# Kernel tuning notes

Hardware: AMD Instinct MI355X
Metric: run time of the kernel (lower is better)

## Reference

```python
import jax, jax.numpy as jnp
import numpy as np

B, S, IN, D, H, FF, L = 16, 1000, 32, 512, 8, 2048, 6
DK = D // H
EPS = 1e-5


def setup_inputs() -> dict:
    key = jax.random.key(0)
    ks = iter(jax.random.split(key, 64))
    def w(shape, s=0.02):
        return jax.random.normal(next(ks), shape, dtype=jnp.float32) * s
    inp = {
        'x': jax.random.normal(next(ks), (B, S, IN), dtype=jnp.float32),
        # input projection
        'Win': w((IN, D)), 'b_in': jnp.zeros((D,), jnp.float32),
        # per-layer attention weights (stacked over L layers)
        'Wq': w((L, D, D)), 'bq': jnp.zeros((L, D), jnp.float32),
        'Wk': w((L, D, D)), 'bk': jnp.zeros((L, D), jnp.float32),
        'Wv': w((L, D, D)), 'bv': jnp.zeros((L, D), jnp.float32),
        'Wo': w((L, D, D)), 'bo': jnp.zeros((L, D), jnp.float32),
        # per-layer feed-forward
        'W1': w((L, D, FF)), 'b1': jnp.zeros((L, FF), jnp.float32),
        'W2': w((L, FF, D)), 'b2': jnp.zeros((L, D), jnp.float32),
        # per-layer layernorms
        'ln1_g': jnp.ones((L, D), jnp.float32), 'ln1_b': jnp.zeros((L, D), jnp.float32),
        'ln2_g': jnp.ones((L, D), jnp.float32), 'ln2_b': jnp.zeros((L, D), jnp.float32),
        # final encoder norm
        'lnf_g': jnp.ones((D,), jnp.float32), 'lnf_b': jnp.zeros((D,), jnp.float32),
        # feature extraction head: D -> D/2 -> D/4
        'Wf1': w((D, D // 2)), 'bf1': jnp.zeros((D // 2,), jnp.float32),
        'Wf2': w((D // 2, D // 4)), 'bf2': jnp.zeros((D // 4,), jnp.float32),
        # reconstruction head: D/4 -> D/2 -> D -> IN
        'Wr1': w((D // 4, D // 2)), 'br1': jnp.zeros((D // 2,), jnp.float32),
        'Wr2': w((D // 2, D)), 'br2': jnp.zeros((D,), jnp.float32),
        'Wr3': w((D, IN)), 'br3': jnp.zeros((IN,), jnp.float32),
        # anomaly head: D/4 -> D/8 -> 1
        'Wa1': w((D // 4, D // 8)), 'ba1': jnp.zeros((D // 8,), jnp.float32),
        'Wa2': w((D // 8, 1)), 'ba2': jnp.zeros((1,), jnp.float32),
    }
    return inp


def _layernorm(x, g, b):
    m = jnp.mean(x, axis=-1, keepdims=True)
    v = jnp.var(x, axis=-1, keepdims=True)
    return (x - m) * jax.lax.rsqrt(v + EPS) * g + b


def _pos_encoding(seq_len, d_model):
    pos = jnp.arange(seq_len, dtype=jnp.float32)[:, None]
    div = jnp.exp(jnp.arange(0, d_model, 2, dtype=jnp.float32) * (-np.log(10000.0) / d_model))
    pe = jnp.zeros((seq_len, d_model), jnp.float32)
    pe = pe.at[:, 0::2].set(jnp.sin(pos * div))
    pe = pe.at[:, 1::2].set(jnp.cos(pos * div))
    return pe


def _encoder(h, Wq, bq, Wk, bk, Wv, bv, Wo, bo, W1, b1, W2, b2,
             ln1_g, ln1_b, ln2_g, ln2_b, lnf_g, lnf_b):
    h = h + _pos_encoding(h.shape[1], D)[None]
    scale = 1.0 / np.sqrt(DK)
    for i in range(L):
        # multi-head self-attention
        q = (h @ Wq[i] + bq[i]).reshape(B, S, H, DK).transpose(0, 2, 1, 3)
        k = (h @ Wk[i] + bk[i]).reshape(B, S, H, DK).transpose(0, 2, 1, 3)
        v = (h @ Wv[i] + bv[i]).reshape(B, S, H, DK).transpose(0, 2, 1, 3)
        scores = jnp.einsum('bhsd,bhtd->bhst', q, k) * scale  # [B,H,S,S]
        attn = jax.nn.softmax(scores, axis=-1)
        ctx = jnp.einsum('bhst,bhtd->bhsd', attn, v)
        ctx = ctx.transpose(0, 2, 1, 3).reshape(B, S, D)
        attn_out = ctx @ Wo[i] + bo[i]
        h = _layernorm(h + attn_out, ln1_g[i], ln1_b[i])
        # feed-forward
        ff = jax.nn.relu(h @ W1[i] + b1[i]) @ W2[i] + b2[i]
        h = _layernorm(h + ff, ln2_g[i], ln2_b[i])
    return _layernorm(h, lnf_g, lnf_b)


def reference(x, Win, b_in, Wq, bq, Wk, bk, Wv, bv, Wo, bo, W1, b1, W2, b2,
              ln1_g, ln1_b, ln2_g, ln2_b, lnf_g, lnf_b,
              Wf1, bf1, Wf2, bf2, Wr1, br1, Wr2, br2, Wr3, br3,
              Wa1, ba1, Wa2, ba2):
    h = x @ Win + b_in  # [B,S,D]
    h = _encoder(h, Wq, bq, Wk, bk, Wv, bv, Wo, bo, W1, b1, W2, b2,
                 ln1_g, ln1_b, ln2_g, ln2_b, lnf_g, lnf_b)
    feat = jax.nn.relu(h @ Wf1 + bf1) @ Wf2 + bf2  # [B,S,D/4]
    recon = jax.nn.relu(jax.nn.relu(feat @ Wr1 + br1) @ Wr2 + br2) @ Wr3 + br3  # [B,S,IN]
    anomaly = jax.nn.sigmoid(jax.nn.relu(feat @ Wa1 + ba1) @ Wa2 + ba2)  # [B,S,1]
    return recon, anomaly
```

## Files before the change

kernel.cpp:

```cpp
#include <hip/hip_runtime.h>
#include <hip/hip_bf16.h>
#include <math.h>

#define B_  16
#define S_  1000
#define IN_ 32
#define D_  512
#define H_  8
#define FF_ 2048
#define L_  6
#define DK_ 64
#define M_  (B_ * S_)
#define SP_ 1024

typedef __bf16 bf16x8 __attribute__((ext_vector_type(8)));
typedef float  floatx4 __attribute__((ext_vector_type(4)));

#define FLAG_RELU 1
#define FLAG_BF16 2
#define FLAG_QKV  4

#define QSCALE 0.18033688011112042f

__device__ __forceinline__ void gll16(const __bf16* g, __bf16* l) {
    __builtin_amdgcn_global_load_lds(
        (const __attribute__((address_space(1))) unsigned int*)g,
        (__attribute__((address_space(3))) unsigned int*)l, 16, 0, 0);
}

__global__ __launch_bounds__(256) void gemm_mfma(
    const __bf16* __restrict__ A, const __bf16* __restrict__ BT,
    const float* __restrict__ bias, void* __restrict__ C,
    int M, int N, int K, int flags)
{
    __shared__ __bf16 Asm[128 * 32];
    __shared__ __bf16 Bsm[128 * 32];

    int tid  = threadIdx.x;
    int wave = tid >> 6;
    int lane = tid & 63;
    int bm = blockIdx.y * 128;
    int bn = blockIdx.x * 128;
    int wm = (wave & 1) * 64;
    int wn = (wave >> 1) * 64;
    int lm = lane & 15;
    int lq = lane >> 4;

    floatx4 acc[4][4] = {};

    int crow  = tid >> 2;
    int cpart = (tid & 3) * 8;
    const __bf16* ag0 = A + (size_t)(bm + crow) * K + cpart;
    const __bf16* ag1 = A + (size_t)(bm + 64 + crow) * K + cpart;
    __bf16* al0 = Asm + tid * 8;
    __bf16* al1 = Asm + 2048 + tid * 8;
    int nr0 = bn + crow, nr1 = bn + 64 + crow;
    const __bf16* bg0 = BT + (size_t)nr0 * K + cpart;
    const __bf16* bg1 = BT + (size_t)nr1 * K + cpart;
    __bf16* bl0 = Bsm + tid * 8;
    __bf16* bl1 = Bsm + 2048 + tid * 8;
    bool bv0 = nr0 < N, bv1 = nr1 < N;

    for (int k0 = 0; k0 < K; k0 += 32) {
        __syncthreads();
        gll16(ag0 + k0, al0);
        gll16(ag1 + k0, al1);
        if (bv0) gll16(bg0 + k0, bl0);
        if (bv1) gll16(bg1 + k0, bl1);
        __syncthreads();

        bf16x8 af[4], bf[4];
        #pragma unroll
        for (int i = 0; i < 4; ++i) {
            af[i] = *(const bf16x8*)&Asm[(wm + i * 16 + lm) * 32 + lq * 8];
            bf[i] = *(const bf16x8*)&Bsm[(wn + i * 16 + lm) * 32 + lq * 8];
        }
        #pragma unroll
        for (int i = 0; i < 4; ++i)
            #pragma unroll
            for (int j = 0; j < 4; ++j)
                acc[i][j] = __builtin_amdgcn_mfma_f32_16x16x32_bf16(
                    af[i], bf[j], acc[i][j], 0, 0, 0);
    }

    if (flags & FLAG_QKV) {
        int sec = bn >> 9;
        if (sec < 2) {
            __bf16* dst = (__bf16*)C + (sec ? (size_t)8192000 : 0);
            #pragma unroll
            for (int j = 0; j < 4; ++j) {
                int col = (bn & 511) + wn + j * 16 + lm;
                float bvv = bias[bn + wn + j * 16 + lm];
                #pragma unroll
                for (int i = 0; i < 4; ++i)
                    #pragma unroll
                    for (int r = 0; r < 4; ++r) {
                        int m = bm + wm + i * 16 + lq * 4 + r;
                        dst[(size_t)m * 512 + col] = (__bf16)(acc[i][j][r] + bvv);
                    }
            }
        } else {
            __bf16* vt = (__bf16*)C + (size_t)16384000;
            int bbq[4], s0[4];
            #pragma unroll
            for (int i = 0; i < 4; ++i) {
                int m0 = bm + wm + i * 16 + lq * 4;
                bbq[i] = m0 / 1000;
                s0[i]  = m0 - bbq[i] * 1000;
            }
            #pragma unroll
            for (int j = 0; j < 4; ++j) {
                int col = (bn & 511) + wn + j * 16 + lm;
                float bvv = bias[bn + wn + j * 16 + lm];
                int head = col >> 6, dk = col & 63;
                #pragma unroll
                for (int i = 0; i < 4; ++i) {
                    __bf16 t4[4];
                    #pragma unroll
                    for (int r = 0; r < 4; ++r) t4[r] = (__bf16)(acc[i][j][r] + bvv);
                    *(uint2*)(vt + ((size_t)(bbq[i] * H_ + head) * DK_ + dk) * SP_ + s0[i])
                        = *(uint2*)t4;
                }
            }
        }
        return;
    }

    #pragma unroll
    for (int j = 0; j < 4; ++j) {
        int n = bn + wn + j * 16 + lm;
        if (n >= N) continue;
        float bv = bias[n];
        #pragma unroll
        for (int i = 0; i < 4; ++i) {
            #pragma unroll
            for (int r = 0; r < 4; ++r) {
                int m = bm + wm + i * 16 + lq * 4 + r;
                float v = acc[i][j][r] + bv;
                if (flags & FLAG_RELU) v = fmaxf(v, 0.f);
                if (flags & FLAG_BF16) ((__bf16*)C)[(size_t)m * N + n] = (__bf16)v;
                else                   ((float*)C)[(size_t)m * N + n] = v;
            }
        }
    }
}

__device__ __forceinline__ void trans_tile(
    const float* __restrict__ src, __bf16* __restrict__ dst,
    int K, int N, float scale, int tx0, int ty0)
{
    __shared__ float t[32][33];
    int n0 = tx0 * 32, k0 = ty0 * 32;
    int tx = threadIdx.x & 31, ty = threadIdx.x >> 5;
    #pragma unroll
    for (int i = 0; i < 32; i += 8) {
        int k = k0 + ty + i, n = n0 + tx;
        t[ty + i][tx] = (k < K && n < N) ? src[(size_t)k * N + n] * scale : 0.f;
    }
    __syncthreads();
    #pragma unroll
    for (int i = 0; i < 32; i += 8) {
        int n = n0 + ty + i, k = k0 + tx;
        if (n < N && k < K) dst[(size_t)n * K + k] = (__bf16)t[tx][ty + i];
    }
}

__global__ __launch_bounds__(256) void transpose_qkvo(
    const float* __restrict__ Wq, const float* __restrict__ Wk,
    const float* __restrict__ Wv, const float* __restrict__ Wo,
    __bf16* __restrict__ WqkvT, __bf16* __restrict__ WoT)
{
    int l = blockIdx.z >> 2, which = blockIdx.z & 3;
    const float* src; __bf16* dst; float sc = 1.f;
    size_t so = (size_t)l * 512 * 512;
    if (which == 0)      { src = Wq + so; dst = WqkvT + (size_t)l * 1536 * 512; sc = QSCALE; }
    else if (which == 1) { src = Wk + so; dst = WqkvT + (size_t)l * 1536 * 512 + 512 * 512; }
    else if (which == 2) { src = Wv + so; dst = WqkvT + (size_t)l * 1536 * 512 + 1024 * 512; }
    else                 { src = Wo + so; dst = WoT + so; }
    trans_tile(src, dst, 512, 512, sc, blockIdx.x, blockIdx.y);
}

__global__ __launch_bounds__(256) void transpose_ffn(
    const float* __restrict__ W1, const float* __restrict__ W2,
    __bf16* __restrict__ W1T, __bf16* __restrict__ W2T)
{
    int l = blockIdx.z >> 1, which = blockIdx.z & 1;
    size_t so = (size_t)l * 512 * 2048;
    int K = which ? 2048 : 512, N = which ? 512 : 2048;
    if ((int)blockIdx.x >= N / 32 || (int)blockIdx.y >= K / 32) return;
    trans_tile((which ? W2 : W1) + so, (which ? W2T : W1T) + so,
               K, N, 1.f, blockIdx.x, blockIdx.y);
}

struct TDesc { const float* src; __bf16* dst; int K; int N; float scale; };
struct TDescArr { TDesc d[7]; };

__global__ __launch_bounds__(256) void transpose_misc(TDescArr ds)
{
    TDesc t = ds.d[blockIdx.z];
    if ((int)blockIdx.x * 32 >= t.N || (int)blockIdx.y * 32 >= t.K) return;
    trans_tile(t.src, t.dst, t.K, t.N, t.scale, blockIdx.x, blockIdx.y);
}

__global__ void cast_bf16(const float* __restrict__ src, __bf16* __restrict__ dst, int n)
{
    int i = blockIdx.x * 256 + threadIdx.x;
    if (i < n) dst[i] = (__bf16)src[i];
}

__global__ void concat_bias(const float* __restrict__ bq, const float* __restrict__ bk,
                            const float* __restrict__ bv, float* __restrict__ dst)
{
    int i = blockIdx.x * 256 + threadIdx.x;
    if (i >= L_ * 1536) return;
    int l = i / 1536, j = i - l * 1536;
    float v = (j < 512) ? bq[l * 512 + j] * QSCALE
            : (j < 1024) ? bk[l * 512 + j - 512]
                         : bv[l * 512 + j - 1024];
    dst[i] = v;
}

__global__ void add_pos_kernel(float* __restrict__ h, __bf16* __restrict__ hb)
{
    int idx = blockIdx.x * 256 + threadIdx.x;
    if (idx >= B_ * S_ * D_) return;
    int d = idx % D_;
    int s = (idx / D_) % S_;
    int two_i = d & ~1;
    float ang = (float)s * expf((float)two_i * (-9.210340371976184f / (float)D_));
    float v = h[idx] + ((d & 1) ? cosf(ang) : sinf(ang));
    h[idx] = v;
    hb[idx] = (__bf16)v;
}

#define AST 72

__global__ __launch_bounds__(256) void attn_mfma(
    const __bf16* __restrict__ q, const __bf16* __restrict__ k,
    const __bf16* __restrict__ vt, __bf16* __restrict__ ctx)
{
    const int qt = blockIdx.x, hh = blockIdx.y, bb = blockIdx.z;
    const int tid = threadIdx.x;
    const int wave = tid >> 6, lane = tid & 63;
    const int lm = lane & 15, lq = lane >> 4;

    __shared__ __bf16 Ks[64 * AST];
    __shared__ __bf16 Vt[64 * AST];
    __shared__ __bf16 Ps[4][32 * AST];

    const size_t headbase = (size_t)bb * S_ * D_ + hh * DK_;
    const __bf16* kbase  = k + headbase;
    const __bf16* vtbase = vt + (size_t)(bb * H_ + hh) * DK_ * SP_;

    bf16x8 af[2][2] = {};
    #pragma unroll
    for (int iq = 0; iq < 2; ++iq) {
        int qrow = qt * 128 + wave * 32 + iq * 16 + lm;
        if (qrow < S_) {
            const __bf16* qp = q + headbase + (size_t)qrow * D_;
            af[iq][0] = *(const bf16x8*)(qp + lq * 8);
            af[iq][1] = *(const bf16x8*)(qp + 32 + lq * 8);
        }
    }

    float lsum[2][4] = {};
    floatx4 oacc[2][4] = {};

    const int sr  = tid >> 3;
    const int sc8 = (tid & 7) * 8;

    uint4 ku[2], vu[2];
    #pragma unroll
    for (int i = 0; i < 2; ++i) {
        int r = sr + i * 32;
        ku[i] = *(const uint4*)(kbase + (size_t)r * D_ + sc8);
        vu[i] = *(const uint4*)(vtbase + (size_t)r * SP_ + sc8);
    }

    for (int jt = 0; jt < 16; ++jt) {
        const int t0 = jt * 64;
        const bool tail = (jt == 15);

        __syncthreads();
        #pragma unroll
        for (int i = 0; i < 2; ++i) {
            int r = sr + i * 32;
            *(uint4*)&Ks[r * AST + sc8] = ku[i];
            *(uint4*)&Vt[r * AST + sc8] = vu[i];
        }
        __syncthreads();

        if (jt < 15) {
            int t0n = t0 + 64;
            #pragma unroll
            for (int i = 0; i < 2; ++i) {
                int r = sr + i * 32;
                int trow = t0n + r;
                ku[i] = (trow < S_) ? *(const uint4*)(kbase + (size_t)trow * D_ + sc8)
                                    : make_uint4(0, 0, 0, 0);
                vu[i] = *(const uint4*)(vtbase + (size_t)r * SP_ + t0n + sc8);
            }
        }

        #pragma unroll
        for (int iq = 0; iq < 2; ++iq) {
            floatx4 sacc[4] = {};
            #pragma unroll
            for (int ks = 0; ks < 2; ++ks)
                #pragma unroll
                for (int jb = 0; jb < 4; ++jb) {
                    bf16x8 bf = *(const bf16x8*)&Ks[(jb * 16 + lm) * AST + ks * 32 + lq * 8];
                    sacc[jb] = __builtin_amdgcn_mfma_f32_16x16x32_bf16(
                        af[iq][ks], bf, sacc[jb], 0, 0, 0);
                }

            __bf16 pb[4][4];
            if (!tail) {
                #pragma unroll
                for (int jb = 0; jb < 4; ++jb)
                    #pragma unroll
                    for (int r = 0; r < 4; ++r) {
                        float p = exp2f(sacc[jb][r]);
                        lsum[iq][r] += p;
                        pb[jb][r] = (__bf16)p;
                    }
            } else {
                #pragma unroll
                for (int jb = 0; jb < 4; ++jb) {
                    bool valid = (t0 + jb * 16 + lm) < S_;
                    #pragma unroll
                    for (int r = 0; r < 4; ++r) {
                        float p = valid ? exp2f(sacc[jb][r]) : 0.f;
                        lsum[iq][r] += p;
                        pb[jb][r] = (__bf16)p;
                    }
                }
            }

            #pragma unroll
            for (int jb = 0; jb < 4; ++jb)
                #pragma unroll
                for (int r = 0; r < 4; ++r)
                    Ps[wave][(iq * 16 + lq * 4 + r) * AST + jb * 16 + lm] = pb[jb][r];

            #pragma unroll
            for (int ks = 0; ks < 2; ++ks) {
                bf16x8 pa = *(const bf16x8*)&Ps[wave][(iq * 16 + lm) * AST + ks * 32 + lq * 8];
                #pragma unroll
                for (int jb = 0; jb < 4; ++jb) {
                    bf16x8 bv = *(const bf16x8*)&Vt[(jb * 16 + lm) * AST + ks * 32 + lq * 8];
                    oacc[iq][jb] = __builtin_amdgcn_mfma_f32_16x16x32_bf16(
                        pa, bv, oacc[iq][jb], 0, 0, 0);
                }
            }
        }
    }

    #pragma unroll
    for (int iq = 0; iq < 2; ++iq) {
        float linv[4];
        #pragma unroll
        for (int r = 0; r < 4; ++r) {
            float l = lsum[iq][r];
            l += __shfl_xor(l, 1, 64);
            l += __shfl_xor(l, 2, 64);
            l += __shfl_xor(l, 4, 64);
            l += __shfl_xor(l, 8, 64);
            linv[r] = 1.f / l;
        }
        #pragma unroll
        for (int jb = 0; jb < 4; ++jb)
            #pragma unroll
            for (int r = 0; r < 4; ++r) {
                int srow = qt * 128 + wave * 32 + iq * 16 + lq * 4 + r;
                if (srow < S_)
                    ctx[headbase + (size_t)srow * D_ + jb * 16 + lm] =
                        (__bf16)(oacc[iq][jb][r] * linv[r]);
            }
    }
}

__global__ __launch_bounds__(256) void ln_kernel(
    const float* __restrict__ x, const __bf16* __restrict__ delta,
    const float* __restrict__ g, const float* __restrict__ b,
    float* __restrict__ out, __bf16* __restrict__ outb, int has_delta)
{
    int row = blockIdx.x;
    int tid = threadIdx.x;
    __shared__ float red[256];

    const size_t base = (size_t)row * D_;
    float v0 = x[base + tid];
    float v1 = x[base + tid + 256];
    if (has_delta) {
        v0 += (float)delta[base + tid];
        v1 += (float)delta[base + tid + 256];
    }
    red[tid] = v0 + v1; __syncthreads();
    for (int o = 128; o > 0; o >>= 1) {
        if (tid < o) red[tid] += red[tid + o];
        __syncthreads();
    }
    float mean = red[0] * (1.f / D_);
    __syncthreads();
    float d0 = v0 - mean, d1 = v1 - mean;
    red[tid] = d0 * d0 + d1 * d1; __syncthreads();
    for (int o = 128; o > 0; o >>= 1) {
        if (tid < o) red[tid] += red[tid + o];
        __syncthreads();
    }
    float rstd = rsqrtf(red[0] * (1.f / D_) + 1e-5f);
    float o0 = d0 * rstd * g[tid]       + b[tid];
    float o1 = d1 * rstd * g[tid + 256] + b[tid + 256];
    out[base + tid]        = o0;
    out[base + tid + 256]  = o1;
    outb[base + tid]       = (__bf16)o0;
    outb[base + tid + 256] = (__bf16)o1;
}

__global__ __launch_bounds__(256) void a2_kernel(
    const float* __restrict__ a1, const float* __restrict__ Wa2,
    const float* __restrict__ ba2, float* __restrict__ out)
{
    int row = blockIdx.x * 4 + (threadIdx.x >> 6);
    int lane = threadIdx.x & 63;
    if (row >= M_) return;
    float p = a1[(size_t)row * 64 + lane] * Wa2[lane];
    for (int o = 32; o > 0; o >>= 1) p += __shfl_down(p, o, 64);
    if (lane == 0) out[row] = 1.f / (1.f + expf(-(p + ba2[0])));
}

extern "C" void kernel_launch(void* const* d_in, const int* in_sizes, int n_in,
                              void* d_out, int out_size, void* d_ws, size_t ws_size,
                              hipStream_t stream)
{
    const float* x     = (const float*)d_in[0];
    const float* Win   = (const float*)d_in[1];
    const float* b_in  = (const float*)d_in[2];
    const float* Wq    = (const float*)d_in[3];
    const float* bq    = (const float*)d_in[4];
    const float* Wk    = (const float*)d_in[5];
    const float* bk    = (const float*)d_in[6];
    const float* Wv    = (const float*)d_in[7];
    const float* bv    = (const float*)d_in[8];
    const float* Wo    = (const float*)d_in[9];
    const float* bo    = (const float*)d_in[10];
    const float* W1    = (const float*)d_in[11];
    const float* b1    = (const float*)d_in[12];
    const float* W2    = (const float*)d_in[13];
    const float* b2    = (const float*)d_in[14];
    const float* ln1_g = (const float*)d_in[15];
    const float* ln1_b = (const float*)d_in[16];
    const float* ln2_g = (const float*)d_in[17];
    const float* ln2_b = (const float*)d_in[18];
    const float* lnf_g = (const float*)d_in[19];
    const float* lnf_b = (const float*)d_in[20];
    const float* Wf1   = (const float*)d_in[21];
    const float* bf1   = (const float*)d_in[22];
    const float* Wf2   = (const float*)d_in[23];
    const float* bf2   = (const float*)d_in[24];
    const float* Wr1   = (const float*)d_in[25];
    const float* br1   = (const float*)d_in[26];
    const float* Wr2   = (const float*)d_in[27];
    const float* br2   = (const float*)d_in[28];
    const float* Wr3   = (const float*)d_in[29];
    const float* br3   = (const float*)d_in[30];
    const float* Wa1   = (const float*)d_in[31];
    const float* ba1   = (const float*)d_in[32];
    const float* Wa2   = (const float*)d_in[33];
    const float* ba2   = (const float*)d_in[34];

    float* recon_out   = (float*)d_out;
    float* anomaly_out = (float*)d_out + (size_t)M_ * IN_;

    char* ws = (char*)d_ws;
    float*  h    = (float*)(ws + 0);
    __bf16* tmpb = (__bf16*)(ws + 32768000);
    __bf16* hb   = (__bf16*)(ws + 65536000);
    __bf16* qb   = (__bf16*)(ws + 81920000);
    __bf16* kb   = (__bf16*)(ws + 98304000);
    __bf16* vtb  = (__bf16*)(ws + 114688000);
    __bf16* ctxb = (__bf16*)(ws + 131465216);
    __bf16* ffmid = qb;

    __bf16* t1b   = (__bf16*)(ws + 81920000);
    __bf16* featb = (__bf16*)(ws + 90112000);
    __bf16* r1b   = (__bf16*)(ws + 94208000);
    __bf16* r2b   = (__bf16*)(ws + 102400000);
    float*  a1b   = (float*)(ws + 118784000);

    size_t woff = 147849216;
    auto alloc_bf = [&](size_t elems) { __bf16* p = (__bf16*)(ws + woff); woff += elems * 2; return p; };
    __bf16* WinT  = alloc_bf(32 * 512);
    __bf16* WqkvT = alloc_bf((size_t)L_ * 1536 * 512);
    __bf16* WoT   = alloc_bf((size_t)L_ * 512 * 512);
    __bf16* W1T   = alloc_bf((size_t)L_ * 512 * 2048);
    __bf16* W2T   = alloc_bf((size_t)L_ * 2048 * 512);
    __bf16* Wf1T  = alloc_bf(512 * 256);
    __bf16* Wf2T  = alloc_bf(256 * 128);
    __bf16* Wr1T  = alloc_bf(128 * 256);
    __bf16* Wr2T  = alloc_bf(256 * 512);
    __bf16* Wr3T  = alloc_bf(512 * 32);
    __bf16* Wa1T  = alloc_bf(128 * 64);
    __bf16* xb    = alloc_bf((size_t)M_ * IN_);
    float*  bqkv  = (float*)(ws + woff);  woff += (size_t)L_ * 1536 * 4;

    dim3 blk(256);
    auto gg = [](int N) { return dim3((N + 127) / 128, M_ / 128); };

    hipLaunchKernelGGL(transpose_qkvo, dim3(16, 16, L_ * 4), blk, 0, stream,
                       Wq, Wk, Wv, Wo, WqkvT, WoT);
    hipLaunchKernelGGL(transpose_ffn, dim3(64, 64, L_ * 2), blk, 0, stream,
                       W1, W2, W1T, W2T);
    TDescArr misc;
    misc.d[0] = {Win, WinT, 32, 512, 1.f};
    misc.d[1] = {Wf1, Wf1T, 512, 256, 1.f};
    misc.d[2] = {Wf2, Wf2T, 256, 128, 1.f};
    misc.d[3] = {Wr1, Wr1T, 128, 256, 1.f};
    misc.d[4] = {Wr2, Wr2T, 256, 512, 1.f};
    misc.d[5] = {Wr3, Wr3T, 512, 32, 1.f};
    misc.d[6] = {Wa1, Wa1T, 128, 64, 1.f};
    hipLaunchKernelGGL(transpose_misc, dim3(16, 16, 7), blk, 0, stream, misc);
    hipLaunchKernelGGL(cast_bf16, dim3((M_ * IN_ + 255) / 256), blk, 0, stream,
                       x, xb, M_ * IN_);
    hipLaunchKernelGGL(concat_bias, dim3((L_ * 1536 + 255) / 256), blk, 0, stream,
                       bq, bk, bv, bqkv);

    hipLaunchKernelGGL(gemm_mfma, gg(D_), blk, 0, stream,
                       xb, WinT, b_in, (void*)h, M_, D_, IN_, 0);
    hipLaunchKernelGGL(add_pos_kernel, dim3((B_ * S_ * D_ + 255) / 256), blk, 0, stream,
                       h, hb);

    for (int l = 0; l < L_; ++l) {
        size_t wo = (size_t)l * 512 * 512;
        size_t fo = (size_t)l * 512 * 2048;

        hipLaunchKernelGGL(gemm_mfma, dim3(12, M_ / 128), blk, 0, stream,
                           hb, WqkvT + (size_t)l * 1536 * 512, bqkv + (size_t)l * 1536,
                           (void*)qb, M_, 1536, 512, FLAG_QKV);

        hipLaunchKernelGGL(attn_mfma, dim3(8, H_, B_), blk, 0, stream,
                           qb, kb, vtb, ctxb);

        hipLaunchKernelGGL(gemm_mfma, gg(D_), blk, 0, stream,
                           ctxb, WoT + wo, bo + (size_t)l * D_, (void*)tmpb, M_, D_, D_,
                           FLAG_BF16);
        hipLaunchKernelGGL(ln_kernel, dim3(M_), blk, 0, stream,
                           h, tmpb, ln1_g + (size_t)l * D_, ln1_b + (size_t)l * D_, h, hb, 1);

        hipLaunchKernelGGL(gemm_mfma, gg(FF_), blk, 0, stream,
                           hb, W1T + fo, b1 + (size_t)l * FF_, (void*)ffmid, M_, FF_, D_,
                           FLAG_RELU | FLAG_BF16);
        hipLaunchKernelGGL(gemm_mfma, gg(D_), blk, 0, stream,
                           ffmid, W2T + fo, b2 + (size_t)l * D_, (void*)tmpb, M_, D_, FF_,
                           FLAG_BF16);
        hipLaunchKernelGGL(ln_kernel, dim3(M_), blk, 0, stream,
                           h, tmpb, ln2_g + (size_t)l * D_, ln2_b + (size_t)l * D_, h, hb, 1);
    }

    hipLaunchKernelGGL(ln_kernel, dim3(M_), blk, 0, stream,
                       h, nullptr, lnf_g, lnf_b, h, hb, 0);

    hipLaunchKernelGGL(gemm_mfma, gg(256), blk, 0, stream,
                       hb, Wf1T, bf1, (void*)t1b, M_, 256, 512, FLAG_RELU | FLAG_BF16);
    hipLaunchKernelGGL(gemm_mfma, gg(128), blk, 0, stream,
                       t1b, Wf2T, bf2, (void*)featb, M_, 128, 256, FLAG_BF16);

    hipLaunchKernelGGL(gemm_mfma, gg(256), blk, 0, stream,
                       featb, Wr1T, br1, (void*)r1b, M_, 256, 128, FLAG_RELU | FLAG_BF16);
    hipLaunchKernelGGL(gemm_mfma, gg(512), blk, 0, stream,
                       r1b, Wr2T, br2, (void*)r2b, M_, 512, 256, FLAG_RELU | FLAG_BF16);
    hipLaunchKernelGGL(gemm_mfma, gg(IN_), blk, 0, stream,
                       r2b, Wr3T, br3, (void*)recon_out, M_, IN_, 512, 0);

    hipLaunchKernelGGL(gemm_mfma, gg(64), blk, 0, stream,
                       featb, Wa1T, ba1, (void*)a1b, M_, 64, 128, FLAG_RELU);
    hipLaunchKernelGGL(a2_kernel, dim3((M_ + 3) / 4), blk, 0, stream,
                       a1b, Wa2, ba2, anomaly_out);
}
```

Baseline: 2.215 ms.

## Keep attention probabilities in registers by computing transposed scores and permuting V

Swaps the MFMA operands so the score tile comes out transposed, letting each lane's exp'd probabilities form the A operand of the PV MFMA directly. This removes the per-wave shared-memory P buffer and its write/read round trip. To line up with that register layout, V^T is stored into LDS with a permuted column order, and the row-sum reduction becomes a cross-lane shuffle over lane groups. The tail-masking condition is rewritten for the new lane-to-key mapping, and the permuted LDS stores use narrower 8-byte writes.

```diff
diff --git a/kernel.cpp b/kernel.cpp
--- a/kernel.cpp
+++ b/kernel.cpp
@@ -246,7 +246,6 @@
 
     __shared__ __bf16 Ks[64 * AST];
     __shared__ __bf16 Vt[64 * AST];
-    __shared__ __bf16 Ps[4][32 * AST];
 
     const size_t headbase = (size_t)bb * S_ * D_ + hh * DK_;
     const __bf16* kbase  = k + headbase;
@@ -263,11 +262,12 @@
         }
     }
 
-    float lsum[2][4] = {};
+    float lsum[2] = {};
     floatx4 oacc[2][4] = {};
 
     const int sr  = tid >> 3;
     const int sc8 = (tid & 7) * 8;
+    const int colA = (sc8 & 32) | ((sc8 & 8) << 1) | ((sc8 & 16) >> 2);
 
     uint4 ku[2], vu[2];
     #pragma unroll
@@ -286,7 +286,10 @@
         for (int i = 0; i < 2; ++i) {
             int r = sr + i * 32;
             *(uint4*)&Ks[r * AST + sc8] = ku[i];
-            *(uint4*)&Vt[r * AST + sc8] = vu[i];
+            uint2 vlo = make_uint2(vu[i].x, vu[i].y);
+            uint2 vhi = make_uint2(vu[i].z, vu[i].w);
+            *(uint2*)&Vt[r * AST + colA]     = vlo;
+            *(uint2*)&Vt[r * AST + colA + 8] = vhi;
         }
         __syncthreads();
 
@@ -309,9 +312,9 @@
             for (int ks = 0; ks < 2; ++ks)
                 #pragma unroll
                 for (int jb = 0; jb < 4; ++jb) {
-                    bf16x8 bf = *(const bf16x8*)&Ks[(jb * 16 + lm) * AST + ks * 32 + lq * 8];
+                    bf16x8 kf = *(const bf16x8*)&Ks[(jb * 16 + lm) * AST + ks * 32 + lq * 8];
                     sacc[jb] = __builtin_amdgcn_mfma_f32_16x16x32_bf16(
-                        af[iq][ks], bf, sacc[jb], 0, 0, 0);
+                        kf, af[iq][ks], sacc[jb], 0, 0, 0);
                 }
 
             __bf16 pb[4][4];
@@ -321,31 +324,27 @@
                     #pragma unroll
                     for (int r = 0; r < 4; ++r) {
                         float p = exp2f(sacc[jb][r]);
-                        lsum[iq][r] += p;
+                        lsum[iq] += p;
                         pb[jb][r] = (__bf16)p;
                     }
             } else {
                 #pragma unroll
-                for (int jb = 0; jb < 4; ++jb) {
-                    bool valid = (t0 + jb * 16 + lm) < S_;
+                for (int jb = 0; jb < 4; ++jb)
                     #pragma unroll
                     for (int r = 0; r < 4; ++r) {
+                        bool valid = (t0 + jb * 16 + lq * 4 + r) < S_;
                         float p = valid ? exp2f(sacc[jb][r]) : 0.f;
-                        lsum[iq][r] += p;
+                        lsum[iq] += p;
                         pb[jb][r] = (__bf16)p;
                     }
-                }
-            }
-
-            #pragma unroll
-            for (int jb = 0; jb < 4; ++jb)
-                #pragma unroll
-                for (int r = 0; r < 4; ++r)
-                    Ps[wave][(iq * 16 + lq * 4 + r) * AST + jb * 16 + lm] = pb[jb][r];
+            }
 
             #pragma unroll
             for (int ks = 0; ks < 2; ++ks) {
-                bf16x8 pa = *(const bf16x8*)&Ps[wave][(iq * 16 + lm) * AST + ks * 32 + lq * 8];
+                bf16x8 pa;
+                #pragma unroll
+                for (int j = 0; j < 8; ++j)
+                    pa[j] = pb[2 * ks + (j >> 2)][j & 3];
                 #pragma unroll
                 for (int jb = 0; jb < 4; ++jb) {
                     bf16x8 bv = *(const bf16x8*)&Vt[(jb * 16 + lm) * AST + ks * 32 + lq * 8];
@@ -358,16 +357,13 @@
 
     #pragma unroll
     for (int iq = 0; iq < 2; ++iq) {
+        float l = lsum[iq];
+        l += __shfl_xor(l, 16, 64);
+        l += __shfl_xor(l, 32, 64);
         float linv[4];
         #pragma unroll
-        for (int r = 0; r < 4; ++r) {
-            float l = lsum[iq][r];
-            l += __shfl_xor(l, 1, 64);
-            l += __shfl_xor(l, 2, 64);
-            l += __shfl_xor(l, 4, 64);
-            l += __shfl_xor(l, 8, 64);
-            linv[r] = 1.f / l;
-        }
+        for (int r = 0; r < 4; ++r)
+            linv[r] = 1.f / __shfl(l, lq * 4 + r, 64);
         #pragma unroll
         for (int jb = 0; jb < 4; ++jb)
             #pragma unroll
```

Result: faster. 2.015 ms (-9.0%).
